# Performance work log

Measured on AMD Instinct MI355X. Metric: run time of the kernel, lower is better.

The kernel has to match this reference:

```python
import jax, jax.numpy as jnp
import numpy as np

# --- Instant-NGP hash-grid constants (from __init__ defaults) ---
T = 2 ** 19          # hash table size per level
NLEVELS = 16
F = 2                # features per level
L = 4                # dir positional-encoding frequencies
LEVELS = np.geomspace(16, 2048, NLEVELS, dtype=int)            # grid resolutions
PRIMES = jnp.array([1, 2654435761, 805459861], dtype=jnp.uint32)
FREQS = (2.0 ** np.arange(L)).astype(np.float32)
# corner c in 0..7 -> bit b_i = use ceil along dim i (matches torch corner order)
BITS = jnp.array([[(c >> i) & 1 for i in range(3)] for c in range(8)], dtype=bool)  # (8,3)


def _hash_encode(pos, table):
    """pos: (P,3) level-scaled positions; table: (T,F). Returns (P,F).
    Spatial hash + gather + trilinear interpolation (== grid_sample trick)."""
    fl = jnp.floor(pos)
    ce = jnp.ceil(pos)
    frac = pos - fl                                             # (P,3) in [0,1)
    corners = jnp.where(BITS[None], ce[:, None, :], fl[:, None, :]).astype(jnp.int32)  # (P,8,3)
    # uint32 wrap-around arithmetic matches torch int64 mod 2^19 (T is a power of 2)
    v = corners.astype(jnp.uint32) * PRIMES                     # (P,8,3)
    h = (v[..., 0] ^ v[..., 1] ^ v[..., 2]) & jnp.uint32(T - 1) # (P,8)
    cf = table[h]                                               # (P,8,F) irregular gather
    w = jnp.prod(jnp.where(BITS[None], frac[:, None, :], 1.0 - frac[:, None, :]), axis=-1)  # (P,8)
    return jnp.einsum('pc,pcf->pf', w, cf)


def setup_inputs() -> dict:
    key = jax.random.key(0)
    ks = jax.random.split(key, 16)
    N, S = 2048, 192
    # positions s.t. x*scene_scale + 0.5 lies mostly in (0,1), a few outside (mask path)
    x = (jax.random.uniform(ks[0], (N, S, 3), jnp.float32) - 0.5) * 1.1
    r_dir = jax.random.normal(ks[1], (N, S, 3), jnp.float32)
    tables = jax.random.normal(ks[2], (NLEVELS, T, F), jnp.float32) * 1e-4

    def lin(k, fan_in, fan_out):
        return jax.random.normal(k, (fan_in, fan_out), jnp.float32) / np.float32(np.sqrt(fan_in))

    din = F * NLEVELS              # 32
    cin = 16 + 3 + 3 * L * 2       # 43
    return {
        'x': x, 'r_dir': r_dir, 'tables': tables,
        'dW1': lin(ks[3], din, 64), 'db1': jnp.zeros((64,), jnp.float32),
        'dW2': lin(ks[4], 64, 16), 'db2': jnp.zeros((16,), jnp.float32),
        'cW1': lin(ks[5], cin, 64), 'cb1': jnp.zeros((64,), jnp.float32),
        'cW2': lin(ks[6], 64, 64), 'cb2': jnp.zeros((64,), jnp.float32),
        'cW3': lin(ks[7], 64, 3), 'cb3': jnp.zeros((3,), jnp.float32),
    }


def reference(x, r_dir, tables, dW1, db1, dW2, db2, cW1, cb1, cW2, cb2, cW3, cb3):
    scene_scale = 1.0
    N, S = x.shape[0], r_dir.shape[1]
    xf = x.reshape(-1, 3) * scene_scale + 0.5          # (P,3)
    rd = r_dir.reshape(-1, 3)                          # (P,3)
    mask = jnp.all(xf > 0, axis=-1) & jnp.all(xf < 1, axis=-1)  # (P,)

    # multi-resolution hash encoding (fixed 16-level loop, vectorized over points)
    feats = jnp.concatenate(
        [_hash_encode(xf * np.float32(LEVELS[i]), tables[i]) for i in range(NLEVELS)],
        axis=-1)                                       # (P, F*NLEVELS)

    log_sigma = jax.nn.relu(feats @ dW1 + db1) @ dW2 + db2        # (P,16)

    # direction positional encoding: [dir, sin(2^l*2pi*dir), cos(...)] -> (P, 3+3*2L)
    xin = rd[..., None] * (2.0 * np.pi * jnp.asarray(FREQS))      # (P,3,L)
    enc = jnp.concatenate([jnp.sin(xin), jnp.cos(xin)], axis=-1).reshape(rd.shape[0], -1)
    enc_dir = jnp.concatenate([rd, enc], axis=-1)                 # (P,27)

    h = jax.nn.relu(jnp.concatenate([log_sigma, enc_dir], axis=-1) @ cW1 + cb1)
    h = jax.nn.relu(h @ cW2 + cb2)
    color = jax.nn.sigmoid(h @ cW3 + cb3)                         # (P,3)

    color = jnp.where(mask[:, None], color, 0.0)
    sigma = jnp.where(mask[:, None], jnp.exp(log_sigma[:, :1]), 0.0)
    return color.reshape(N, S, 3), sigma.reshape(N, S, 1)
```

## Files before the change

kernel.cpp:

```cpp
#include <hip/hip_runtime.h>
#include <hip/hip_bf16.h>
#include <cstdint>

#define NPTS (2048 * 192)
#define TBL  (1u << 19)
#define TMASK (TBL - 1u)
#define PBLOCKS (NPTS / 256)
#define ENC_BLOCKS (PBLOCKS * 16)
#define PREP_BLOCKS 6
#define PE_BLOCKS PBLOCKS
#define MLP_BLOCKS 3072
#define P2 2654435761u
#define P3 805459861u

__constant__ float LVLS[16] = {16.f, 22.f, 30.f, 42.f, 58.f, 80.f, 111.f, 153.f,
                               212.f, 294.f, 406.f, 561.f, 776.f, 1072.f, 1482.f, 2048.f};

__device__ __forceinline__ uint32_t f2bf(float f) {
    uint32_t u = __float_as_uint(f);
    return (u + 0x7FFFu + ((u >> 16) & 1u)) >> 16;
}
__device__ __forceinline__ uint32_t pack2(float a, float b) {
    return f2bf(a) | (f2bf(b) << 16);
}
__device__ __forceinline__ uint32_t pack2t(float a, float b) {
    return __builtin_amdgcn_perm(__float_as_uint(b), __float_as_uint(a),
                                 0x07060302u);
}

#if __has_builtin(__builtin_amdgcn_sinf)
#define SIN_REV(x) __builtin_amdgcn_sinf(x)
#else
#define SIN_REV(x) __sinf(6.28318530717958647f * (x))
#endif

typedef __attribute__((ext_vector_type(8))) short bf16x8;
typedef __attribute__((ext_vector_type(4))) float f32x4;

#define MFMA_BF16 __builtin_amdgcn_mfma_f32_16x16x32_bf16

__device__ __forceinline__ float pe_val(int r, float rx, float ry, float rz)
{
    int t = r - 19;
    int d = t >> 3;
    int s = t & 7;
    float comp = (d == 0) ? rx : ((d == 1) ? ry : rz);
    float a = ldexpf(comp, s & 3) + ((s >= 4) ? 0.25f : 0.0f);
    float v = SIN_REV(a);
    if (r == 16) v = rx;
    if (r == 17) v = ry;
    if (r == 18) v = rz;
    if (r == 43) v = 1.0f;
    if (r > 43)  v = 0.0f;
    return v;
}

__global__ __launch_bounds__(256) void k_encode(const float* __restrict__ x,
                                                const float* __restrict__ tables,
                                                uint32_t* __restrict__ feats,
                                                const float* __restrict__ dW1,
                                                const float* __restrict__ dW2,
                                                const float* __restrict__ cW1,
                                                const float* __restrict__ cb1,
                                                const float* __restrict__ cW2,
                                                const float* __restrict__ cW3,
                                                uint4* __restrict__ wfrags,
                                                const float* __restrict__ rdir,
                                                uint32_t* __restrict__ dirs)
{
    if (blockIdx.x >= ENC_BLOCKS + PREP_BLOCKS) {
        int p = (blockIdx.x - ENC_BLOCKS - PREP_BLOCKS) * 256 + threadIdx.x;
        size_t p3 = (size_t)p * 3;
        float rx = rdir[p3 + 0], ry = rdir[p3 + 1], rz = rdir[p3 + 2];
#pragma unroll
        for (int i = 0; i < 14; ++i)
            dirs[(size_t)i * NPTS + p] =
                pack2t(pe_val(16 + 2 * i, rx, ry, rz),
                       pe_val(17 + 2 * i, rx, ry, rz));
        return;
    }
    if (blockIdx.x >= ENC_BLOCKS) {
        int t = (blockIdx.x - ENC_BLOCKS) * 256 + threadIdx.x;
        if (t >= 24 * 64) return;
        int frag = t >> 6, lane = t & 63;
        const float* W; const float* bfold = nullptr;
        int OUT, Kact, Mact, k0, m0;
        if (frag < 4)       { W = dW1; OUT = 64; Kact = 32; Mact = 64; k0 = 0;               m0 = frag * 16; }
        else if (frag < 6)  { W = dW2; OUT = 16; Kact = 64; Mact = 16; k0 = (frag - 4) * 32; m0 = 0; }
        else if (frag < 14) { int i = frag - 6;  W = cW1; OUT = 64; Kact = 43; Mact = 64;
                              k0 = (i & 1) * 32; m0 = (i >> 1) * 16; bfold = cb1; }
        else if (frag < 22) { int i = frag - 14; W = cW2; OUT = 64; Kact = 64; Mact = 64;
                              k0 = (i & 1) * 32; m0 = (i >> 1) * 16; }
        else                { W = cW3; OUT = 3;  Kact = 64; Mact = 3;  k0 = (frag - 22) * 32; m0 = 0; }
        int m  = m0 + (lane & 15);
        int kq = k0 + ((lane >> 4) << 3);
        uint32_t d[4];
#pragma unroll
        for (int j = 0; j < 4; ++j) {
            float a0 = 0.f, a1 = 0.f;
            int ka = kq + 2 * j, kb = ka + 1;
            if (m < Mact) {
                a0 = (ka < Kact) ? W[(size_t)ka * OUT + m]
                                 : ((bfold && ka == Kact) ? bfold[m] : 0.f);
                a1 = (kb < Kact) ? W[(size_t)kb * OUT + m]
                                 : ((bfold && kb == Kact) ? bfold[m] : 0.f);
            }
            d[j] = f2bf(a0) | (f2bf(a1) << 16);
        }
        wfrags[t] = make_uint4(d[0], d[1], d[2], d[3]);
        return;
    }

    int xs   = blockIdx.x & 7;
    int i    = blockIdx.x >> 3;
    int half = i / PBLOCKS;
    int pb   = i - half * PBLOCKS;
    int lvl  = xs + (half << 3);
    int p    = pb * 256 + threadIdx.x;

    size_t p3 = (size_t)p * 3;
    float x0 = x[p3 + 0] + 0.5f;
    float x1 = x[p3 + 1] + 0.5f;
    float x2 = x[p3 + 2] + 0.5f;
    size_t oidx = (size_t)lvl * NPTS + p;

    bool m = (x0 > 0.f) && (x0 < 1.f) && (x1 > 0.f) && (x1 < 1.f) &&
             (x2 > 0.f) && (x2 < 1.f);
    if (!m) { feats[oidx] = 0u; return; }

    float s  = LVLS[lvl];
    float px = x0 * s, py = x1 * s, pz = x2 * s;
    float flx = floorf(px), fly = floorf(py), flz = floorf(pz);
    float frx = px - flx,   fry = py - fly,   frz = pz - flz;
    int ix = (int)flx, iy = (int)fly, iz = (int)flz;
    uint32_t ux = (uint32_t)ix, uy = (uint32_t)iy, uz = (uint32_t)iz;

    uint32_t base[4];
    base[0] = (uy * P2) ^ (uz * P3);
    base[1] = ((uy + 1u) * P2) ^ (uz * P3);
    base[2] = (uy * P2) ^ ((uz + 1u) * P3);
    base[3] = ((uy + 1u) * P2) ^ ((uz + 1u) * P3);

    const float2* tb = (const float2*)tables + (size_t)lvl * TBL;

    float2 v[8];
    if ((ix & 1) == 0) {
        const float4* tb4 = (const float4*)tb;
#pragma unroll
        for (int cc = 0; cc < 4; ++cc) {
            uint32_t h0 = (base[cc] ^ ux) & TMASK;
            float4 qv = tb4[h0 >> 1];
            bool hi = (h0 & 1u) != 0u;
            float2 e0 = hi ? make_float2(qv.z, qv.w) : make_float2(qv.x, qv.y);
            float2 e1 = hi ? make_float2(qv.x, qv.y) : make_float2(qv.z, qv.w);
            v[(cc << 1)]     = e0;
            v[(cc << 1) | 1] = e1;
        }
    } else {
        uint32_t h[8];
#pragma unroll
        for (int c = 0; c < 8; ++c)
            h[c] = (base[c >> 1] ^ (ux + (uint32_t)(c & 1))) & TMASK;
#pragma unroll
        for (int c = 0; c < 8; ++c) v[c] = tb[h[c]];
    }

    float f0 = 0.f, f1 = 0.f;
#pragma unroll
    for (int c = 0; c < 8; ++c) {
        float w = ((c & 1)        ? frx : 1.f - frx)
                * (((c >> 1) & 1) ? fry : 1.f - fry)
                * (((c >> 2) & 1) ? frz : 1.f - frz);
        f0 += w * v[c].x;
        f1 += w * v[c].y;
    }
    feats[oidx] = pack2(f0, f1);
}

__device__ __forceinline__ void quad_gather(uint32_t x, uint32_t& e02, uint32_t& e13)
{
    uint32_t u = x, v = x;
    asm("v_permlane32_swap_b32 %0, %1" : "+v"(u), "+v"(v));
    asm("v_permlane16_swap_b32 %0, %1" : "+v"(u), "+v"(v));
    e02 = u; e13 = v;
}

__device__ __forceinline__ bf16x8 trans_frag(uint32_t p01a, uint32_t p23a,
                                             uint32_t p01b, uint32_t p23b, bool hi)
{
    uint32_t a02, a13, c02, c13, b02, b13, e02, e13;
    quad_gather(p01a, a02, a13);
    quad_gather(p23a, c02, c13);
    quad_gather(p01b, b02, b13);
    quad_gather(p23b, e02, e13);
    union { bf16x8 v; uint32_t d[4]; } u;
    u.d[0] = hi ? b02 : a02;
    u.d[1] = hi ? e02 : c02;
    u.d[2] = hi ? b13 : a13;
    u.d[3] = hi ? e13 : c13;
    return u.v;
}

__device__ __forceinline__ bf16x8 trans_frag1(uint32_t p01, uint32_t p23)
{
    uint32_t a02, a13, c02, c13;
    quad_gather(p01, a02, a13);
    quad_gather(p23, c02, c13);
    union { bf16x8 v; uint32_t d[4]; } u;
    u.d[0] = a02;
    u.d[1] = c02;
    u.d[2] = a13;
    u.d[3] = c13;
    return u.v;
}

__global__ __launch_bounds__(256, 4) void k_mlp(const uint32_t* __restrict__ feats,
                                                const uint4* __restrict__ wfrags,
                                                const float* __restrict__ x,
                                                const uint32_t* __restrict__ dirs,
                                                const float* __restrict__ db1,
                                                const float* __restrict__ db2,
                                                const float* __restrict__ cb2,
                                                const float* __restrict__ cb3,
                                                float* __restrict__ out)
{
    __shared__ uint4 wlds[24 * 64];
#pragma unroll
    for (int t = 0; t < 6; ++t)
        wlds[t * 256 + threadIdx.x] = wfrags[t * 256 + threadIdx.x];

    int lane = threadIdx.x & 63;
    int q = lane >> 4, col = lane & 15;
    bool hi = q >= 2;
    int wgid = blockIdx.x * 4 + (threadIdx.x >> 6);

    float4 b1v[4], c2v[4];
#pragma unroll
    for (int mt = 0; mt < 4; ++mt) {
        b1v[mt] = *(const float4*)&db1[mt * 16 + q * 4];
        c2v[mt] = *(const float4*)&cb2[mt * 16 + q * 4];
    }
    float4 b2v = *(const float4*)&db2[q * 4];
    float cb30 = cb3[0], cb31 = cb3[1], cb32 = cb3[2];

    __syncthreads();

#define LDW(f) ({ union { uint4 u_; bf16x8 v_; } w_; w_.u_ = wlds[(f) * 64 + lane]; w_.v_; })

#pragma unroll
    for (int it = 0; it < 2; ++it) {
        int g = (wgid * 2 + it) << 4;
        int pt = g + col;
        size_t pt3 = (size_t)pt * 3;

        union { bf16x8 v; uint32_t d[4]; } Bf;
#pragma unroll
        for (int w = 0; w < 4; ++w)
            Bf.d[w] = feats[(size_t)(q * 4 + w) * NPTS + g + col];

        uint32_t da[4], dbv[4];
#pragma unroll
        for (int j = 0; j < 4; ++j) {
            int pa = ((q - 2) * 4 + j) & 7;
            da[j] = dirs[(size_t)pa * NPTS + pt];
            int pb = 8 + q * 4 + j;
            pb = (pb > 13) ? 13 : pb;
            dbv[j] = dirs[(size_t)pb * NPTS + pt];
        }

        f32x4 T[4];
#pragma unroll
        for (int mt = 0; mt < 4; ++mt) {
            f32x4 c; c[0] = b1v[mt].x; c[1] = b1v[mt].y; c[2] = b1v[mt].z; c[3] = b1v[mt].w;
            T[mt] = MFMA_BF16(LDW(mt), Bf.v, c, 0, 0, 0);
        }
        uint32_t p01[4], p23[4];
#pragma unroll
        for (int mt = 0; mt < 4; ++mt) {
            p01[mt] = pack2t(fmaxf(T[mt][0], 0.f), fmaxf(T[mt][1], 0.f));
            p23[mt] = pack2t(fmaxf(T[mt][2], 0.f), fmaxf(T[mt][3], 0.f));
        }
        bf16x8 Bh0 = trans_frag(p01[0], p23[0], p01[1], p23[1], hi);
        bf16x8 Bh1 = trans_frag(p01[2], p23[2], p01[3], p23[3], hi);

        f32x4 Dls;
        {
            f32x4 c; c[0] = b2v.x; c[1] = b2v.y; c[2] = b2v.z; c[3] = b2v.w;
            Dls = MFMA_BF16(LDW(4), Bh0, c, 0, 0, 0);
            Dls = MFMA_BF16(LDW(5), Bh1, Dls, 0, 0, 0);
        }
        uint32_t lp01 = pack2t(Dls[0], Dls[1]);
        uint32_t lp23 = pack2t(Dls[2], Dls[3]);

        union { bf16x8 v; uint32_t d[4]; } Ba0, Ba1;
        Ba0.v = trans_frag1(lp01, lp23);
#pragma unroll
        for (int j = 0; j < 4; ++j) {
            Ba0.d[j] = (q >= 2) ? da[j] : Ba0.d[j];
            bool vld = (q == 0) | ((q == 1) & (j < 2));
            Ba1.d[j] = vld ? dbv[j] : 0u;
        }

        f32x4 C1[4];
#pragma unroll
        for (int mt = 0; mt < 4; ++mt) {
            f32x4 c = {0.f, 0.f, 0.f, 0.f};
            c = MFMA_BF16(LDW(6 + 2 * mt), Ba0.v, c, 0, 0, 0);
            C1[mt] = MFMA_BF16(LDW(7 + 2 * mt), Ba1.v, c, 0, 0, 0);
        }
#pragma unroll
        for (int mt = 0; mt < 4; ++mt) {
            p01[mt] = pack2t(fmaxf(C1[mt][0], 0.f), fmaxf(C1[mt][1], 0.f));
            p23[mt] = pack2t(fmaxf(C1[mt][2], 0.f), fmaxf(C1[mt][3], 0.f));
        }
        bf16x8 Bc0 = trans_frag(p01[0], p23[0], p01[1], p23[1], hi);
        bf16x8 Bc1 = trans_frag(p01[2], p23[2], p01[3], p23[3], hi);

        f32x4 C2[4];
#pragma unroll
        for (int mt = 0; mt < 4; ++mt) {
            f32x4 c; c[0] = c2v[mt].x; c[1] = c2v[mt].y; c[2] = c2v[mt].z; c[3] = c2v[mt].w;
            c = MFMA_BF16(LDW(14 + 2 * mt), Bc0, c, 0, 0, 0);
            C2[mt] = MFMA_BF16(LDW(15 + 2 * mt), Bc1, c, 0, 0, 0);
        }
#pragma unroll
        for (int mt = 0; mt < 4; ++mt) {
            p01[mt] = pack2t(fmaxf(C2[mt][0], 0.f), fmaxf(C2[mt][1], 0.f));
            p23[mt] = pack2t(fmaxf(C2[mt][2], 0.f), fmaxf(C2[mt][3], 0.f));
        }
        bf16x8 Bd0 = trans_frag(p01[0], p23[0], p01[1], p23[1], hi);
        bf16x8 Bd1 = trans_frag(p01[2], p23[2], p01[3], p23[3], hi);

        f32x4 c5 = {0.f, 0.f, 0.f, 0.f};
        if (q == 0) { c5[0] = cb30; c5[1] = cb31; c5[2] = cb32; }
        f32x4 Dc = MFMA_BF16(LDW(22), Bd0, c5, 0, 0, 0);
        Dc = MFMA_BF16(LDW(23), Bd1, Dc, 0, 0, 0);

        if (q == 0) {
            float xfx = x[pt3 + 0] + 0.5f;
            float xfy = x[pt3 + 1] + 0.5f;
            float xfz = x[pt3 + 2] + 0.5f;
            bool m = (xfx > 0.f) && (xfx < 1.f) && (xfy > 0.f) && (xfy < 1.f) &&
                     (xfz > 0.f) && (xfz < 1.f);
            out[pt3 + 0] = m ? 1.f / (1.f + __expf(-Dc[0])) : 0.f;
            out[pt3 + 1] = m ? 1.f / (1.f + __expf(-Dc[1])) : 0.f;
            out[pt3 + 2] = m ? 1.f / (1.f + __expf(-Dc[2])) : 0.f;
            out[(size_t)3 * NPTS + pt] = m ? __expf(Dls[0]) : 0.f;
        }
    }
#undef LDW
}

extern "C" void kernel_launch(void* const* d_in, const int* in_sizes, int n_in,
                              void* d_out, int out_size, void* d_ws, size_t ws_size,
                              hipStream_t stream) {
    const float* x      = (const float*)d_in[0];
    const float* rdir   = (const float*)d_in[1];
    const float* tables = (const float*)d_in[2];
    const float* dW1 = (const float*)d_in[3];
    const float* db1 = (const float*)d_in[4];
    const float* dW2 = (const float*)d_in[5];
    const float* db2 = (const float*)d_in[6];
    const float* cW1 = (const float*)d_in[7];
    const float* cb1 = (const float*)d_in[8];
    const float* cW2 = (const float*)d_in[9];
    const float* cb2 = (const float*)d_in[10];
    const float* cW3 = (const float*)d_in[11];
    const float* cb3 = (const float*)d_in[12];
    float* out = (float*)d_out;

    uint4*    wfrags = (uint4*)d_ws;
    uint32_t* feats  = (uint32_t*)((char*)d_ws + 32768);
    uint32_t* dirs   = (uint32_t*)((char*)d_ws + 32768 + (size_t)16 * NPTS * 4);

    k_encode<<<ENC_BLOCKS + PREP_BLOCKS + PE_BLOCKS, 256, 0, stream>>>(
        x, tables, feats, dW1, dW2, cW1, cb1, cW2, cW3, wfrags, rdir, dirs);
    k_mlp<<<MLP_BLOCKS, 256, 0, stream>>>(feats, wfrags, x, dirs,
                                          db1, db2, cb2, cb3, out);
}
```

Before: 241.7 us.

## Stage point coords via coalesced float4 LDS loads; keep MLP weights in registers

```diff
diff --git a/kernel.cpp b/kernel.cpp
--- a/kernel.cpp
+++ b/kernel.cpp
@@ -68,10 +68,17 @@
                                                 const float* __restrict__ rdir,
                                                 uint32_t* __restrict__ dirs)
 {
+    __shared__ float sx[768];
+
     if (blockIdx.x >= ENC_BLOCKS + PREP_BLOCKS) {
-        int p = (blockIdx.x - ENC_BLOCKS - PREP_BLOCKS) * 256 + threadIdx.x;
-        size_t p3 = (size_t)p * 3;
-        float rx = rdir[p3 + 0], ry = rdir[p3 + 1], rz = rdir[p3 + 2];
+        int pbt = blockIdx.x - ENC_BLOCKS - PREP_BLOCKS;
+        if (threadIdx.x < 192)
+            *(float4*)&sx[threadIdx.x * 4] =
+                ((const float4*)rdir)[(size_t)pbt * 192 + threadIdx.x];
+        __syncthreads();
+        int p = pbt * 256 + threadIdx.x;
+        int t3 = threadIdx.x * 3;
+        float rx = sx[t3 + 0], ry = sx[t3 + 1], rz = sx[t3 + 2];
 #pragma unroll
         for (int i = 0; i < 14; ++i)
             dirs[(size_t)i * NPTS + p] =
@@ -118,10 +125,14 @@
     int lvl  = xs + (half << 3);
     int p    = pb * 256 + threadIdx.x;
 
-    size_t p3 = (size_t)p * 3;
-    float x0 = x[p3 + 0] + 0.5f;
-    float x1 = x[p3 + 1] + 0.5f;
-    float x2 = x[p3 + 2] + 0.5f;
+    if (threadIdx.x < 192)
+        *(float4*)&sx[threadIdx.x * 4] =
+            ((const float4*)x)[(size_t)pb * 192 + threadIdx.x];
+    __syncthreads();
+    int t3 = threadIdx.x * 3;
+    float x0 = sx[t3 + 0] + 0.5f;
+    float x1 = sx[t3 + 1] + 0.5f;
+    float x2 = sx[t3 + 2] + 0.5f;
     size_t oidx = (size_t)lvl * NPTS + p;
 
     bool m = (x0 > 0.f) && (x0 < 1.f) && (x1 > 0.f) && (x1 < 1.f) &&
@@ -214,26 +225,37 @@
     return u.v;
 }
 
-__global__ __launch_bounds__(256, 4) void k_mlp(const uint32_t* __restrict__ feats,
-                                                const uint4* __restrict__ wfrags,
-                                                const float* __restrict__ x,
-                                                const uint32_t* __restrict__ dirs,
-                                                const float* __restrict__ db1,
-                                                const float* __restrict__ db2,
-                                                const float* __restrict__ cb2,
-                                                const float* __restrict__ cb3,
-                                                float* __restrict__ out)
-{
-    __shared__ uint4 wlds[24 * 64];
-#pragma unroll
-    for (int t = 0; t < 6; ++t)
-        wlds[t * 256 + threadIdx.x] = wfrags[t * 256 + threadIdx.x];
-
+__global__ __launch_bounds__(256) void k_mlp(const uint32_t* __restrict__ feats,
+                                             const uint4* __restrict__ wfrags,
+                                             const float* __restrict__ x,
+                                             const uint32_t* __restrict__ dirs,
+                                             const float* __restrict__ db1,
+                                             const float* __restrict__ db2,
+                                             const float* __restrict__ cb2,
+                                             const float* __restrict__ cb3,
+                                             float* __restrict__ out)
+{
     int lane = threadIdx.x & 63;
     int q = lane >> 4, col = lane & 15;
     bool hi = q >= 2;
     int wgid = blockIdx.x * 4 + (threadIdx.x >> 6);
 
+    union { bf16x8 v; uint4 u; } wf;
+    bf16x8 A1[4], A2[2], A3[4][2], A4[4][2], A5[2];
+#pragma unroll
+    for (int mt = 0; mt < 4; ++mt) { wf.u = wfrags[(0 + mt) * 64 + lane]; A1[mt] = wf.v; }
+#pragma unroll
+    for (int kt = 0; kt < 2; ++kt) { wf.u = wfrags[(4 + kt) * 64 + lane]; A2[kt] = wf.v; }
+#pragma unroll
+    for (int mt = 0; mt < 4; ++mt)
+#pragma unroll
+        for (int kt = 0; kt < 2; ++kt) {
+            wf.u = wfrags[(6 + 2 * mt + kt) * 64 + lane];  A3[mt][kt] = wf.v;
+            wf.u = wfrags[(14 + 2 * mt + kt) * 64 + lane]; A4[mt][kt] = wf.v;
+        }
+#pragma unroll
+    for (int kt = 0; kt < 2; ++kt) { wf.u = wfrags[(22 + kt) * 64 + lane]; A5[kt] = wf.v; }
+
     float4 b1v[4], c2v[4];
 #pragma unroll
     for (int mt = 0; mt < 4; ++mt) {
@@ -242,10 +264,6 @@
     }
     float4 b2v = *(const float4*)&db2[q * 4];
     float cb30 = cb3[0], cb31 = cb3[1], cb32 = cb3[2];
-
-    __syncthreads();
-
-#define LDW(f) ({ union { uint4 u_; bf16x8 v_; } w_; w_.u_ = wlds[(f) * 64 + lane]; w_.v_; })
 
 #pragma unroll
     for (int it = 0; it < 2; ++it) {
@@ -272,7 +290,7 @@
 #pragma unroll
         for (int mt = 0; mt < 4; ++mt) {
             f32x4 c; c[0] = b1v[mt].x; c[1] = b1v[mt].y; c[2] = b1v[mt].z; c[3] = b1v[mt].w;
-            T[mt] = MFMA_BF16(LDW(mt), Bf.v, c, 0, 0, 0);
+            T[mt] = MFMA_BF16(A1[mt], Bf.v, c, 0, 0, 0);
         }
         uint32_t p01[4], p23[4];
 #pragma unroll
@@ -286,8 +304,8 @@
         f32x4 Dls;
         {
             f32x4 c; c[0] = b2v.x; c[1] = b2v.y; c[2] = b2v.z; c[3] = b2v.w;
-            Dls = MFMA_BF16(LDW(4), Bh0, c, 0, 0, 0);
-            Dls = MFMA_BF16(LDW(5), Bh1, Dls, 0, 0, 0);
+            Dls = MFMA_BF16(A2[0], Bh0, c, 0, 0, 0);
+            Dls = MFMA_BF16(A2[1], Bh1, Dls, 0, 0, 0);
         }
         uint32_t lp01 = pack2t(Dls[0], Dls[1]);
         uint32_t lp23 = pack2t(Dls[2], Dls[3]);
@@ -305,8 +323,8 @@
 #pragma unroll
         for (int mt = 0; mt < 4; ++mt) {
             f32x4 c = {0.f, 0.f, 0.f, 0.f};
-            c = MFMA_BF16(LDW(6 + 2 * mt), Ba0.v, c, 0, 0, 0);
-            C1[mt] = MFMA_BF16(LDW(7 + 2 * mt), Ba1.v, c, 0, 0, 0);
+            c = MFMA_BF16(A3[mt][0], Ba0.v, c, 0, 0, 0);
+            C1[mt] = MFMA_BF16(A3[mt][1], Ba1.v, c, 0, 0, 0);
         }
 #pragma unroll
         for (int mt = 0; mt < 4; ++mt) {
@@ -320,8 +338,8 @@
 #pragma unroll
         for (int mt = 0; mt < 4; ++mt) {
             f32x4 c; c[0] = c2v[mt].x; c[1] = c2v[mt].y; c[2] = c2v[mt].z; c[3] = c2v[mt].w;
-            c = MFMA_BF16(LDW(14 + 2 * mt), Bc0, c, 0, 0, 0);
-            C2[mt] = MFMA_BF16(LDW(15 + 2 * mt), Bc1, c, 0, 0, 0);
+            c = MFMA_BF16(A4[mt][0], Bc0, c, 0, 0, 0);
+            C2[mt] = MFMA_BF16(A4[mt][1], Bc1, c, 0, 0, 0);
         }
 #pragma unroll
         for (int mt = 0; mt < 4; ++mt) {
@@ -333,8 +351,8 @@
 
         f32x4 c5 = {0.f, 0.f, 0.f, 0.f};
         if (q == 0) { c5[0] = cb30; c5[1] = cb31; c5[2] = cb32; }
-        f32x4 Dc = MFMA_BF16(LDW(22), Bd0, c5, 0, 0, 0);
-        Dc = MFMA_BF16(LDW(23), Bd1, Dc, 0, 0, 0);
+        f32x4 Dc = MFMA_BF16(A5[0], Bd0, c5, 0, 0, 0);
+        Dc = MFMA_BF16(A5[1], Bd1, Dc, 0, 0, 0);
 
         if (q == 0) {
             float xfx = x[pt3 + 0] + 0.5f;
@@ -348,7 +366,6 @@
             out[(size_t)3 * NPTS + pt] = m ? __expf(Dls[0]) : 0.f;
         }
     }
-#undef LDW
 }
 
 extern "C" void kernel_launch(void* const* d_in, const int* in_sizes, int n_in,
```

Result: slower. 252.7 us (+4.5%).
